# Kernel tuning notes

Hardware: AMD Instinct MI355X
Metric: run time of the kernel (lower is better)

Reference implementation:

```python
import jax, jax.numpy as jnp
import numpy as np

B, T, D_IN, H, L = 64, 1024, 256, 512, 2

def setup_inputs() -> dict:
    key = jax.random.key(0)
    k1, k2, k3 = jax.random.split(key, 3)
    x = jax.random.normal(k1, (B, T, D_IN), dtype=jnp.float32)
    # Xavier-ish scaled weights; forget-gate bias initialized to 1 as in the module
    W0 = jax.random.normal(k2, (4 * H, D_IN + H), dtype=jnp.float32) * (1.0 / np.sqrt(D_IN + H))
    W1 = jax.random.normal(k3, (4 * H, H + H), dtype=jnp.float32) * (1.0 / np.sqrt(2 * H))
    b0 = jnp.zeros((4 * H,), dtype=jnp.float32).at[H:2 * H].set(1.0)
    b1 = jnp.zeros((4 * H,), dtype=jnp.float32).at[H:2 * H].set(1.0)
    return {"x": x, "W0": W0, "b0": b0, "W1": W1, "b1": b1}

def _cell(x_t, h_prev, c_prev, W, b):
    # combined: (B, H + D); gates: (B, 4H) in order [i, f, g, o]
    combined = jnp.concatenate([h_prev, x_t], axis=1)
    gates = combined @ W.T + b
    i_g, f_g, g_g, o_g = jnp.split(gates, 4, axis=1)
    c_t = jax.nn.sigmoid(f_g) * c_prev + jax.nn.sigmoid(i_g) * jnp.tanh(g_g)
    h_t = jax.nn.sigmoid(o_g) * jnp.tanh(c_t)
    return h_t, c_t

def reference(x, W0, b0, W1, b1):
    batch = x.shape[0]
    hidden = W0.shape[0] // 4
    z = jnp.zeros((batch, hidden), dtype=x.dtype)
    init = (z, z, z, z)  # (h0, c0, h1, c1)

    def step(carry, x_t):
        h0, c0, h1, c1 = carry
        h0, c0 = _cell(x_t, h0, c0, W0, b0)
        h1, c1 = _cell(h0, h1, c1, W1, b1)
        return (h0, c0, h1, c1), h1

    xs = jnp.swapaxes(x, 0, 1)  # (T, B, D)
    (h0, c0, h1, c1), ys = jax.lax.scan(step, init, xs)
    outputs = jnp.swapaxes(ys, 0, 1)  # (B, T, H)
    h_n = jnp.stack([h0, h1], axis=0)  # (L, B, H)
    c_n = jnp.stack([c0, c1], axis=0)
    return outputs, h_n, c_n
```

## Files before the change

kernel.cpp:

```cpp
#include <hip/hip_runtime.h>


#define BB   64
#define TT   1024
#define DIN  256
#define HH   512
#define K0   768
#define K1   1024
#define NTHR 512

typedef float f32x4 __attribute__((ext_vector_type(4)));
typedef short short8 __attribute__((ext_vector_type(8)));
typedef unsigned uint4v __attribute__((ext_vector_type(4)));

union S8U4 { short8 s; unsigned u[4]; };
union RawU { unsigned u[8]; uint4v q[2]; f32x4 v[2]; };

__device__ __forceinline__ void splitf(float f, short& h, short& l) {
    const unsigned u = __float_as_uint(f);
    const float fh = __uint_as_float(u & 0xffff0000u);
    h = (short)(u >> 16);
    l = (short)(__float_as_uint(f - fh) >> 16);
}

__device__ __forceinline__ void split8(f32x4 a, f32x4 b, short8& hi, short8& lo) {
#pragma unroll
    for (int j = 0; j < 4; ++j) {
        short h0, l0, h1, l1;
        splitf(a[j], h0, l0);
        splitf(b[j], h1, l1);
        hi[j] = h0; lo[j] = l0;
        hi[j + 4] = h1; lo[j + 4] = l1;
    }
}

__device__ __forceinline__ unsigned packhl(float f) {
    const unsigned u = __float_as_uint(f);
    const float fh = __uint_as_float(u & 0xffff0000u);
    const unsigned l = __float_as_uint(f - fh) >> 16;
    return (u >> 16) | (l << 16);
}

#define LDX4(dst, ptr, off) \
    asm volatile("global_load_dwordx4 %0, %1, off offset:" #off " sc1" \
                 : "=v"(dst) : "v"(ptr) : "memory")

#define LD2(A, R) do { \
    LDX4((R).q[0], (A), 0);  LDX4((R).q[1], (A), 1024); \
} while (0)

__device__ __forceinline__ void load_x(const float* __restrict__ x, int t,
                                       int nbase, int lm, int kbase, int quad,
                                       RawU raw[4]) {
#pragma unroll
    for (int ks = 0; ks < 4; ++ks) {
        const int kb = kbase + ks * 32;
        if (kb < K0) {
            const int k0 = kb + quad * 8;
            const int bg = nbase + lm;
            const float* p = x + ((size_t)bg * TT + t) * DIN + (k0 - HH);
            raw[ks].v[0] = *(const f32x4*)p;
            raw[ks].v[1] = *(const f32x4*)(p + 4);
        }
    }
}

__global__ __launch_bounds__(NTHR, 2) void lstm_fused(
    const float* __restrict__ x,
    const float* __restrict__ W0, const float* __restrict__ b0v,
    const float* __restrict__ W1, const float* __restrict__ b1v,
    float* __restrict__ out, unsigned* __restrict__ hws, unsigned* __restrict__ bar)
{
    __shared__ float Red[8][64][20];
    __shared__ float biasl[64];

    const int tid   = threadIdx.x;
    const int bid   = blockIdx.x;
    const int layer = bid >> 7;
    const int mgrp  = (bid & 127) >> 2;
    const int g     = bid & 3;
    const int hbase = mgrp << 4;
    const int nbase = g << 4;

    const float* Wm = layer ? W1 : W0;
    const float* bv = layer ? b1v : b0v;
    const int K     = layer ? K1 : K0;

    unsigned* HP0 = hws;
    unsigned* HP1 = hws + 2 * BB * HH;
    unsigned* fOwn = bar + g * 64 + layer * 32;
    unsigned* fOth = bar + g * 64 + (1 - layer) * 32;

    if (tid < 64)
        biasl[tid] = bv[(tid >> 4) * HH + hbase + (tid & 15)];

    const int w     = tid >> 6;
    const int lane  = tid & 63;
    const int quad  = lane >> 4;
    const int lm    = lane & 15;
    const int kbase = w << 7;
    const bool isx  = (!layer && kbase >= HH);
    const bool ish  = (layer || kbase < HH);

    short8 whi[4][4], wlo[4][4];
#pragma unroll
    for (int mt = 0; mt < 4; ++mt)
#pragma unroll
        for (int ks = 0; ks < 4; ++ks) {
            short8 hi = {0, 0, 0, 0, 0, 0, 0, 0};
            short8 lo = {0, 0, 0, 0, 0, 0, 0, 0};
            const int kb = kbase + ks * 32;
            if (kb < K) {
                const int k0 = kb + quad * 8;
                const int r  = mt * 16 + lm;
                const int grow = (r >> 4) * HH + hbase + (r & 15);
                const float* p = Wm + (size_t)grow * K + k0;
                split8(*(const f32x4*)p, *(const f32x4*)(p + 4), hi, lo);
            }
            whi[mt][ks] = hi; wlo[mt][ks] = lo;
        }
    __syncthreads();

    float creg = 0.0f;
    const size_t YOFF = (size_t)BB * TT * HH;

    RawU raw[4];
    if (isx) load_x(x, 0, nbase, lm, kbase, quad, raw);

    for (int t = 0; t < TT; ++t) {
        {
            const int own_tgt = t;
            const int oth_tgt = layer ? (t + 1) : (t - 1);
            if (tid < 32) {
                while ((int)__hip_atomic_load(&fOwn[tid], __ATOMIC_RELAXED,
                                              __HIP_MEMORY_SCOPE_AGENT) < own_tgt)
                    __builtin_amdgcn_s_sleep(1);
            } else if (tid >= 64 && tid < 96) {
                while ((int)__hip_atomic_load(&fOth[tid - 64], __ATOMIC_RELAXED,
                                              __HIP_MEMORY_SCOPE_AGENT) < oth_tgt)
                    __builtin_amdgcn_s_sleep(1);
            }
            __syncthreads();
        }
        const unsigned rpar = (unsigned)((t + 1) & 1) * (BB * HH);
        const unsigned cpar = (unsigned)(t & 1) * (BB * HH);

        if (ish) {
            const unsigned* src; int kk;
            if (kbase < HH) { src = (layer ? HP1 : HP0) + rpar; kk = kbase; }
            else            { src = HP0 + cpar; kk = kbase - HH; }
            const char* A = (const char*)src + ((size_t)kk << 8)
                          + (quad << 11) + ((nbase + lm) << 4);
            LD2(A,         raw[0]);
            LD2(A + 8192,  raw[1]);
            LD2(A + 16384, raw[2]);
            LD2(A + 24576, raw[3]);
        }
        asm volatile("s_waitcnt vmcnt(0)" ::: "memory");
        __builtin_amdgcn_sched_barrier(0);

        f32x4 acc[4];
#pragma unroll
        for (int mt = 0; mt < 4; ++mt) acc[mt] = (f32x4){0.f, 0.f, 0.f, 0.f};

#pragma unroll
        for (int ks = 0; ks < 4; ++ks) {
            const int kb = kbase + ks * 32;
            if (kb < K) {
                short8 chi, clo;
                if (isx) {
                    split8(raw[ks].v[0], raw[ks].v[1], chi, clo);
                } else {
                    S8U4 hi, lo;
#pragma unroll
                    for (int j2 = 0; j2 < 4; ++j2) {
                        const unsigned u0 = raw[ks].u[2 * j2];
                        const unsigned u1 = raw[ks].u[2 * j2 + 1];
                        hi.u[j2] = __builtin_amdgcn_perm(u1, u0, 0x05040100u);
                        lo.u[j2] = __builtin_amdgcn_perm(u1, u0, 0x07060302u);
                    }
                    chi = hi.s; clo = lo.s;
                }
#pragma unroll
                for (int mt = 0; mt < 4; ++mt) {
                    acc[mt] = __builtin_amdgcn_mfma_f32_16x16x32_bf16(whi[mt][ks], chi, acc[mt], 0, 0, 0);
                    acc[mt] = __builtin_amdgcn_mfma_f32_16x16x32_bf16(whi[mt][ks], clo, acc[mt], 0, 0, 0);
                    acc[mt] = __builtin_amdgcn_mfma_f32_16x16x32_bf16(wlo[mt][ks], chi, acc[mt], 0, 0, 0);
                }
            }
        }

#pragma unroll
        for (int mt = 0; mt < 4; ++mt)
#pragma unroll
            for (int r = 0; r < 4; ++r)
                Red[w][mt * 16 + quad * 4 + r][lm] = acc[mt][r];
        __syncthreads();

        float hdef = 0.0f, cdef = 0.0f;
        if (tid < 256) {
            const int b  = tid >> 4;
            const int hh = tid & 15;
            float gsum[4];
#pragma unroll
            for (int g4 = 0; g4 < 4; ++g4) {
                float sgate = biasl[g4 * 16 + hh];
#pragma unroll
                for (int ww = 0; ww < 8; ++ww)
                    sgate += Red[ww][g4 * 16 + hh][b];
                gsum[g4] = sgate;
            }
            const float si = 1.0f / (1.0f + __expf(-gsum[0]));
            const float sf = 1.0f / (1.0f + __expf(-gsum[1]));
            const float so = 1.0f / (1.0f + __expf(-gsum[3]));
            const float c  = sf * creg + si * tanhf(gsum[2]);
            creg = c;
            const float h  = so * tanhf(c);
            hdef = h; cdef = c;
            const int hidx  = hbase + hh;
            const int bglob = nbase + b;
            const unsigned widx = cpar + (((unsigned)hidx >> 2) << 8)
                                + ((unsigned)bglob << 2) + (hidx & 3);
            __hip_atomic_store(&(layer ? HP1 : HP0)[widx], packhl(h),
                               __ATOMIC_RELAXED, __HIP_MEMORY_SCOPE_AGENT);
        }
        __syncthreads();

        if (tid == 0) {
            asm volatile("s_waitcnt vmcnt(0)" ::: "memory");
            __hip_atomic_store(&fOwn[mgrp], (unsigned)(t + 1),
                               __ATOMIC_RELAXED, __HIP_MEMORY_SCOPE_AGENT);
        }
        if (tid < 256) {
            const int b = tid >> 4, hh = tid & 15;
            const int bglob = nbase + b, hidx = hbase + hh;
            if (layer)
                out[((size_t)bglob * TT + t) * HH + hidx] = hdef;
            if (t == TT - 1) {
                if (layer == 0) {
                    out[YOFF + (size_t)bglob * HH + hidx] = hdef;
                    out[YOFF + 2 * BB * HH + (size_t)bglob * HH + hidx] = cdef;
                } else {
                    out[YOFF + BB * HH + (size_t)bglob * HH + hidx] = hdef;
                    out[YOFF + 3 * BB * HH + (size_t)bglob * HH + hidx] = cdef;
                }
            }
        }
        if (isx && t + 1 < TT)
            load_x(x, t + 1, nbase, lm, kbase, quad, raw);
    }
}

extern "C" void kernel_launch(void* const* d_in, const int* in_sizes, int n_in,
                              void* d_out, int out_size, void* d_ws, size_t ws_size,
                              hipStream_t stream) {
    (void)in_sizes; (void)n_in; (void)out_size; (void)ws_size;
    const float* x  = (const float*)d_in[0];
    const float* W0 = (const float*)d_in[1];
    const float* b0 = (const float*)d_in[2];
    const float* W1 = (const float*)d_in[3];
    const float* b1 = (const float*)d_in[4];
    float* out = (float*)d_out;
    unsigned* hws = (unsigned*)d_ws;
    unsigned* bar = (unsigned*)((char*)d_ws + 2 * 2 * 64 * 512 * sizeof(unsigned));

    hipMemsetAsync(d_ws, 0, 2 * 2 * 64 * 512 * sizeof(unsigned) + 4096, stream);

    void* args[] = { (void*)&x, (void*)&W0, (void*)&b0, (void*)&W1, (void*)&b1,
                     (void*)&out, (void*)&hws, (void*)&bar };
    hipLaunchCooperativeKernel(reinterpret_cast<const void*>(lstm_fused),
                               dim3(256), dim3(512), args, 0u, stream);
}
```

Baseline: 4.672 ms.

## Replace per-step flag barriers with tagged h-state ring buffer validation

Adds a 3- or 4-slot ring buffer for hidden states, selected by workspace size. Each stored packed h value carries a 3-bit timestep tag in its low-part mantissa bits, so consumers poll the data itself instead of waiting on per-step flag barriers, and the post-store syncthreads and flag store are dropped. Layer 1 publishes its progress so layer 0 does not overrun the ring, and the Red buffer is double-buffered so one __syncthreads per step can be removed. The tag bits perturb the low-precision residual of h, and the spin loops have bailout limits that could silently read stale data.

```diff
diff --git a/kernel.cpp b/kernel.cpp
--- a/kernel.cpp
+++ b/kernel.cpp
@@ -8,6 +8,7 @@
 #define K0   768
 #define K1   1024
 #define NTHR 512
+#define SL   (BB * HH)
 
 typedef float f32x4 __attribute__((ext_vector_type(4)));
 typedef short short8 __attribute__((ext_vector_type(8)));
@@ -44,10 +45,24 @@
 #define LDX4(dst, ptr, off) \
     asm volatile("global_load_dwordx4 %0, %1, off offset:" #off " sc1" \
                  : "=v"(dst) : "v"(ptr) : "memory")
-
-#define LD2(A, R) do { \
-    LDX4((R).q[0], (A), 0);  LDX4((R).q[1], (A), 1024); \
-} while (0)
+#define LD2(A, R) do { LDX4((R).q[0], (A), 0); LDX4((R).q[1], (A), 1024); } while (0)
+
+__device__ __forceinline__ void load_h(const char* A, RawU raw[4]) {
+    LD2(A,         raw[0]);
+    LD2(A + 8192,  raw[1]);
+    LD2(A + 16384, raw[2]);
+    LD2(A + 24576, raw[3]);
+}
+
+__device__ __forceinline__ unsigned tagbad(const RawU raw[4], unsigned etag16) {
+    unsigned bad = 0;
+#pragma unroll
+    for (int ks = 0; ks < 4; ++ks)
+#pragma unroll
+        for (int j = 0; j < 8; ++j)
+            bad |= (raw[ks].u[j] ^ etag16) & 0x00070000u;
+    return bad;
+}
 
 __device__ __forceinline__ void load_x(const float* __restrict__ x, int t,
                                        int nbase, int lm, int kbase, int quad,
@@ -69,9 +84,10 @@
     const float* __restrict__ x,
     const float* __restrict__ W0, const float* __restrict__ b0v,
     const float* __restrict__ W1, const float* __restrict__ b1v,
-    float* __restrict__ out, unsigned* __restrict__ hws, unsigned* __restrict__ bar)
+    float* __restrict__ out, unsigned* __restrict__ hws,
+    unsigned* __restrict__ bar, int ring)
 {
-    __shared__ float Red[8][64][20];
+    __shared__ float Red[2][8][64][20];
     __shared__ float biasl[64];
 
     const int tid   = threadIdx.x;
@@ -87,9 +103,8 @@
     const int K     = layer ? K1 : K0;
 
     unsigned* HP0 = hws;
-    unsigned* HP1 = hws + 2 * BB * HH;
-    unsigned* fOwn = bar + g * 64 + layer * 32;
-    unsigned* fOth = bar + g * 64 + (1 - layer) * 32;
+    unsigned* HP1 = hws + (unsigned)(ring ? ring : 2) * SL;
+    const unsigned fidx = ((unsigned)layer << 7) + ((unsigned)g << 5);
 
     if (tid < 64)
         biasl[tid] = bv[(tid >> 4) * HH + hbase + (tid & 15)];
@@ -99,7 +114,7 @@
     const int quad  = lane >> 4;
     const int lm    = lane & 15;
     const int kbase = w << 7;
-    const bool isx  = (!layer && kbase >= HH);
+    const bool isx  = (!layer && kbase >= HH && kbase < K0);
     const bool ish  = (layer || kbase < HH);
 
     short8 whi[4][4], wlo[4][4];
@@ -128,36 +143,67 @@
     if (isx) load_x(x, 0, nbase, lm, kbase, quad, raw);
 
     for (int t = 0; t < TT; ++t) {
-        {
+        if (!ring) {
             const int own_tgt = t;
             const int oth_tgt = layer ? (t + 1) : (t - 1);
+            const unsigned oidx = ((unsigned)(1 - layer) << 7) + ((unsigned)g << 5);
             if (tid < 32) {
-                while ((int)__hip_atomic_load(&fOwn[tid], __ATOMIC_RELAXED,
+                while ((int)__hip_atomic_load(&bar[fidx + tid], __ATOMIC_RELAXED,
                                               __HIP_MEMORY_SCOPE_AGENT) < own_tgt)
                     __builtin_amdgcn_s_sleep(1);
             } else if (tid >= 64 && tid < 96) {
-                while ((int)__hip_atomic_load(&fOth[tid - 64], __ATOMIC_RELAXED,
+                while ((int)__hip_atomic_load(&bar[oidx + (tid - 64)], __ATOMIC_RELAXED,
                                               __HIP_MEMORY_SCOPE_AGENT) < oth_tgt)
                     __builtin_amdgcn_s_sleep(1);
             }
             __syncthreads();
         }
-        const unsigned rpar = (unsigned)((t + 1) & 1) * (BB * HH);
-        const unsigned cpar = (unsigned)(t & 1) * (BB * HH);
-
+
+        unsigned rslot, cslot;
+        if (ring == 4)      { rslot = (t + 3) & 3; cslot = t & 3; }
+        else if (ring == 3) { rslot = (t + 2) % 3; cslot = t % 3; }
+        else                { rslot = (t + 1) & 1; cslot = t & 1; }
+
+        const char* A = nullptr;
+        bool val0c = false;
         if (ish) {
             const unsigned* src; int kk;
-            if (kbase < HH) { src = (layer ? HP1 : HP0) + rpar; kk = kbase; }
-            else            { src = HP0 + cpar; kk = kbase - HH; }
-            const char* A = (const char*)src + ((size_t)kk << 8)
-                          + (quad << 11) + ((nbase + lm) << 4);
-            LD2(A,         raw[0]);
-            LD2(A + 8192,  raw[1]);
-            LD2(A + 16384, raw[2]);
-            LD2(A + 24576, raw[3]);
+            if (kbase < HH) { src = (layer ? HP1 : HP0) + rslot * SL; kk = kbase; }
+            else            { src = HP0 + cslot * SL; kk = kbase - HH; val0c = true; }
+            A = (const char*)src + ((size_t)kk << 8) + (quad << 11) + ((nbase + lm) << 4);
+            load_h(A, raw);
+        }
+        if (ring && !layer && w == 0) {
+            const int tgt = t - (ring - 1);
+            if (tgt > 0) {
+                const unsigned gbase = 128u + ((unsigned)g << 5);
+                int spins = 0;
+                while (true) {
+                    const unsigned f = __hip_atomic_load(&bar[gbase + (lane & 31)],
+                                           __ATOMIC_RELAXED, __HIP_MEMORY_SCOPE_AGENT);
+                    if (!__any((int)f < tgt)) break;
+                    if (++spins > 1000000) break;
+                    __builtin_amdgcn_s_sleep(8);
+                }
+            }
         }
         asm volatile("s_waitcnt vmcnt(0)" ::: "memory");
         __builtin_amdgcn_sched_barrier(0);
+
+        if (ring && ish && (val0c || t >= 1)) {
+            const unsigned etag16 =
+                (unsigned)((val0c ? (t % 7) : ((t + 6) % 7)) + 1) << 16;
+            unsigned bad = tagbad(raw, etag16);
+            int spins = 0;
+            while (__any((int)bad)) {
+                if (++spins > 4000) break;
+                __builtin_amdgcn_s_sleep(1);
+                load_h(A, raw);
+                asm volatile("s_waitcnt vmcnt(0)" ::: "memory");
+                __builtin_amdgcn_sched_barrier(0);
+                bad = tagbad(raw, etag16);
+            }
+        }
 
         f32x4 acc[4];
 #pragma unroll
@@ -190,14 +236,19 @@
             }
         }
 
+        const int rb = t & 1;
 #pragma unroll
         for (int mt = 0; mt < 4; ++mt)
 #pragma unroll
             for (int r = 0; r < 4; ++r)
-                Red[w][mt * 16 + quad * 4 + r][lm] = acc[mt][r];
+                Red[rb][w][mt * 16 + quad * 4 + r][lm] = acc[mt][r];
         __syncthreads();
 
-        float hdef = 0.0f, cdef = 0.0f;
+        if (ring && layer && tid == 0)
+            __hip_atomic_store(&bar[fidx + mgrp], (unsigned)(t + 1),
+                               __ATOMIC_RELAXED, __HIP_MEMORY_SCOPE_AGENT);
+
+        float hdef = 0.0f;
         if (tid < 256) {
             const int b  = tid >> 4;
             const int hh = tid & 15;
@@ -207,7 +258,7 @@
                 float sgate = biasl[g4 * 16 + hh];
 #pragma unroll
                 for (int ww = 0; ww < 8; ++ww)
-                    sgate += Red[ww][g4 * 16 + hh][b];
+                    sgate += Red[rb][ww][g4 * 16 + hh][b];
                 gsum[g4] = sgate;
             }
             const float si = 1.0f / (1.0f + __expf(-gsum[0]));
@@ -216,34 +267,39 @@
             const float c  = sf * creg + si * tanhf(gsum[2]);
             creg = c;
             const float h  = so * tanhf(c);
-            hdef = h; cdef = c;
+            hdef = h;
             const int hidx  = hbase + hh;
             const int bglob = nbase + b;
-            const unsigned widx = cpar + (((unsigned)hidx >> 2) << 8)
+            const unsigned widx = (((unsigned)hidx >> 2) << 8)
                                 + ((unsigned)bglob << 2) + (hidx & 3);
-            __hip_atomic_store(&(layer ? HP1 : HP0)[widx], packhl(h),
+            unsigned packed = packhl(h);
+            if (ring)
+                packed = (packed & 0xFFF8FFFFu) | ((unsigned)((t % 7) + 1) << 16);
+            __hip_atomic_store(&(layer ? HP1 : HP0)[cslot * SL + widx], packed,
                                __ATOMIC_RELAXED, __HIP_MEMORY_SCOPE_AGENT);
-        }
-        __syncthreads();
-
-        if (tid == 0) {
-            asm volatile("s_waitcnt vmcnt(0)" ::: "memory");
-            __hip_atomic_store(&fOwn[mgrp], (unsigned)(t + 1),
-                               __ATOMIC_RELAXED, __HIP_MEMORY_SCOPE_AGENT);
-        }
-        if (tid < 256) {
-            const int b = tid >> 4, hh = tid & 15;
-            const int bglob = nbase + b, hidx = hbase + hh;
-            if (layer)
-                out[((size_t)bglob * TT + t) * HH + hidx] = hdef;
+            if (ring && layer)
+                out[((size_t)bglob * TT + t) * HH + hidx] = h;
             if (t == TT - 1) {
                 if (layer == 0) {
-                    out[YOFF + (size_t)bglob * HH + hidx] = hdef;
-                    out[YOFF + 2 * BB * HH + (size_t)bglob * HH + hidx] = cdef;
+                    out[YOFF + (size_t)bglob * HH + hidx] = h;
+                    out[YOFF + 2 * BB * HH + (size_t)bglob * HH + hidx] = c;
                 } else {
-                    out[YOFF + BB * HH + (size_t)bglob * HH + hidx] = hdef;
-                    out[YOFF + 3 * BB * HH + (size_t)bglob * HH + hidx] = cdef;
+                    out[YOFF + BB * HH + (size_t)bglob * HH + hidx] = h;
+                    out[YOFF + 3 * BB * HH + (size_t)bglob * HH + hidx] = c;
                 }
+            }
+        }
+
+        if (!ring) {
+            __syncthreads();
+            if (tid == 0) {
+                asm volatile("s_waitcnt vmcnt(0)" ::: "memory");
+                __hip_atomic_store(&bar[fidx + mgrp], (unsigned)(t + 1),
+                                   __ATOMIC_RELAXED, __HIP_MEMORY_SCOPE_AGENT);
+            }
+            if (layer && tid < 256) {
+                const int b = tid >> 4, hh = tid & 15;
+                out[((size_t)(nbase + b) * TT + t) * HH + hbase + hh] = hdef;
             }
         }
         if (isx && t + 1 < TT)
@@ -254,7 +310,7 @@
 extern "C" void kernel_launch(void* const* d_in, const int* in_sizes, int n_in,
                               void* d_out, int out_size, void* d_ws, size_t ws_size,
                               hipStream_t stream) {
-    (void)in_sizes; (void)n_in; (void)out_size; (void)ws_size;
+    (void)in_sizes; (void)n_in; (void)out_size;
     const float* x  = (const float*)d_in[0];
     const float* W0 = (const float*)d_in[1];
     const float* b0 = (const float*)d_in[2];
@@ -262,12 +318,20 @@
     const float* b1 = (const float*)d_in[4];
     float* out = (float*)d_out;
     unsigned* hws = (unsigned*)d_ws;
-    unsigned* bar = (unsigned*)((char*)d_ws + 2 * 2 * 64 * 512 * sizeof(unsigned));
-
-    hipMemsetAsync(d_ws, 0, 2 * 2 * 64 * 512 * sizeof(unsigned) + 4096, stream);
+
+    const size_t b4 = (size_t)8 * SL * 4 + 4096;
+    const size_t b3 = (size_t)6 * SL * 4 + 4096;
+    const size_t b0sz = (size_t)4 * SL * 4 + 4096;
+    int ring; size_t clr;
+    if (ws_size >= b4)      { ring = 4; clr = b4; }
+    else if (ws_size >= b3) { ring = 3; clr = b3; }
+    else                    { ring = 0; clr = b0sz; }
+    unsigned* bar = (unsigned*)((char*)d_ws + clr - 4096);
+
+    hipMemsetAsync(d_ws, 0, clr, stream);
 
     void* args[] = { (void*)&x, (void*)&W0, (void*)&b0, (void*)&W1, (void*)&b1,
-                     (void*)&out, (void*)&hws, (void*)&bar };
+                     (void*)&out, (void*)&hws, (void*)&bar, (void*)&ring };
     hipLaunchCooperativeKernel(reinterpret_cast<const void*>(lstm_fused),
                                dim3(256), dim3(512), args, 0u, stream);
 }
```

Result: faster. 3.963 ms (-15.2%).
